# Kernel tuning notes

Measured on AMD Instinct MI355X. Metric: run time of the kernel, lower is better.

Reference implementation:

```python
import jax, jax.numpy as jnp
import numpy as np

D, E, N, DD, K = 1024, 2048, 16, 64, 4  # d_model, d_inner, d_state, dt_rank, d_conv
B, L = 2, 1024
EPS = 1e-5


def setup_inputs() -> dict:
    key = jax.random.key(0)
    ks = jax.random.split(key, 12)
    f = lambda k, s, scale=0.02: (jax.random.normal(k, s, jnp.float32) * scale)
    return dict(
        resid=jax.random.normal(ks[0], (B, L, D), jnp.float32),
        workplace_h=jnp.zeros((B, E, N), jnp.float32),
        norm_w=jnp.ones((D,), jnp.float32),
        skip_w=f(ks[1], (E, D)),
        in_w=f(ks[2], (E, D)),
        conv_w=f(ks[3], (E, 1, K), 0.2),
        conv_b=jnp.zeros((E,), jnp.float32),
        wd1=f(ks[4], (DD, E)),
        wd2_w=f(ks[5], (E, DD)),
        wd2_b=jnp.zeros((E,), jnp.float32),
        wb=f(ks[6], (N, E)),
        wc=f(ks[7], (N, E)),
        A_log=f(ks[8], (E, N), 1.0),
        W_D=jnp.ones((E,), jnp.float32),
        out_w=f(ks[9], (D, E)),
    )


def reference(resid, workplace_h, norm_w, skip_w, in_w, conv_w, conv_b,
              wd1, wd2_w, wd2_b, wb, wc, A_log, W_D, out_w):
    # RMSNorm
    x = resid * jax.lax.rsqrt(jnp.mean(resid ** 2, -1, keepdims=True) + EPS) * norm_w
    skip = x @ skip_w.T                      # [B,L,E]
    xi = x @ in_w.T                          # [B,L,E]
    # depthwise causal conv1d (torch pads both sides then slices to L; equivalent to left-pad K-1)
    xc = jnp.swapaxes(xi, 1, 2)              # [B,E,L]
    xc = jax.lax.conv_general_dilated(
        xc, conv_w, window_strides=(1,), padding=[(K - 1, 0)],
        feature_group_count=E, dimension_numbers=('NCH', 'OIH', 'NCH'))
    xc = xc + conv_b[None, :, None]
    x2 = jax.nn.silu(jnp.swapaxes(xc, 1, 2))  # [B,L,E]

    A = -jnp.exp(A_log)                       # [E,N]
    delta = jax.nn.softplus((x2 @ wd1.T) @ wd2_w.T + wd2_b)   # [B,L,E]
    A_bar = jnp.exp(delta[..., None] * A)                      # [B,L,E,N]
    Bm = x2 @ wb.T                                             # [B,L,N]
    B_bar = delta[..., None] * Bm[:, :, None, :]               # [B,L,E,N]
    Cm = x2 @ wc.T                                             # [B,L,N]

    def step(h, inp):
        a, b_, xl, cl = inp                   # [B,E,N],[B,E,N],[B,E],[B,N]
        h = a * h + b_ * xl[..., None]
        y = jnp.einsum('ben,bn->be', h, cl)
        return h, y

    h0 = jnp.zeros_like(workplace_h)          # workplace_h is zeroed (h[:] = 0)
    xs = (jnp.swapaxes(A_bar, 0, 1), jnp.swapaxes(B_bar, 0, 1),
          jnp.swapaxes(x2, 0, 1), jnp.swapaxes(Cm, 0, 1))
    _, ys = jax.lax.scan(step, h0, xs)        # ys: [L,B,E]
    y = jnp.swapaxes(ys, 0, 1)                # [B,L,E]

    y = (y + x2 * W_D) * jax.nn.silu(skip)
    return resid + y @ out_w.T
```

## Files before the change

### kernel.cpp

```cpp
#include <hip/hip_runtime.h>
#include <math.h>

#define Dm 1024
#define Em 2048
#define Nm 16
#define DDm 64
#define Bb 2
#define Lm 1024
#define Mrows (Bb*Lm)
#define NCH 32
#define CLEN 32
#define KS 16
#define KSO 4

typedef __attribute__((ext_vector_type(8))) short bf16x8;
typedef __attribute__((ext_vector_type(4))) float f32x4;
typedef unsigned int u32;
typedef unsigned short u16;

__device__ __forceinline__ u16 f2bf(float f) {
    union { float f; u32 u; } v; v.f = f;
    u32 r = v.u + 0x7fffu + ((v.u >> 16) & 1u);
    return (u16)(r >> 16);
}

__device__ __forceinline__ void async_copy16(const void* g, void* l) {
    __builtin_amdgcn_global_load_lds(
        (const __attribute__((address_space(1))) u32*)g,
        (__attribute__((address_space(3))) u32*)l,
        16, 0, 0);
}

__global__ __launch_bounds__(256) void rmsnorm_kernel(const float* __restrict__ resid,
                                                      const float* __restrict__ w,
                                                      u16* __restrict__ x) {
    int row = blockIdx.x;
    const float* r = resid + (size_t)row * Dm;
    float s = 0.f;
    for (int i = threadIdx.x; i < Dm; i += 256) { float v = r[i]; s += v * v; }
    __shared__ float red[4];
    for (int off = 32; off; off >>= 1) s += __shfl_down(s, off, 64);
    if ((threadIdx.x & 63) == 0) red[threadIdx.x >> 6] = s;
    __syncthreads();
    if (threadIdx.x == 0) {
        float t = red[0] + red[1] + red[2] + red[3];
        red[0] = rsqrtf(t / (float)Dm + 1e-5f);
    }
    __syncthreads();
    float sc = red[0];
    u16* xo = x + (size_t)row * Dm;
    for (int i = threadIdx.x; i < Dm; i += 256) xo[i] = f2bf(r[i] * sc * w[i]);
}

__global__ __launch_bounds__(256) void prep_all_kernel(const float* __restrict__ skip_w,
                                                       const float* __restrict__ in_w,
                                                       const float* __restrict__ out_w,
                                                       const float* __restrict__ wd2_w,
                                                       const float* __restrict__ wb,
                                                       const float* __restrict__ wc,
                                                       const float* __restrict__ wd1,
                                                       u16* __restrict__ skip_w_bf,
                                                       u16* __restrict__ in_w_bf,
                                                       u16* __restrict__ out_w_bf,
                                                       u16* __restrict__ wd2_bf,
                                                       u16* __restrict__ wtb) {
    const int R0 = 2097152, R1 = 4194304, R2 = 6291456, R3 = 6422528, R4 = 6684672;
    int i = blockIdx.x * 256 + threadIdx.x;
    if (i < R0) skip_w_bf[i] = f2bf(skip_w[i]);
    else if (i < R1) in_w_bf[i - R0] = f2bf(in_w[i - R0]);
    else if (i < R2) out_w_bf[i - R1] = f2bf(out_w[i - R1]);
    else if (i < R3) wd2_bf[i - R2] = f2bf(wd2_w[i - R2]);
    else if (i < R4) {
        int j = i - R3;
        int c = j >> 11, k = j & 2047;
        float v = 0.f;
        if (c < 16) v = wb[(size_t)c * Em + k];
        else if (c < 32) v = wc[(size_t)(c - 16) * Em + k];
        else if (c < 96) v = wd1[(size_t)(c - 32) * Em + k];
        wtb[j] = f2bf(v);
    }
}

__global__ __launch_bounds__(256) void gemm64(const u16* __restrict__ A,
                                              const u16* __restrict__ W,
                                              const float* __restrict__ bias,
                                              const float* __restrict__ addend,
                                              float* __restrict__ C,
                                              float* __restrict__ C2, int split,
                                              int M, int N, int lda, int klen, int act) {
    __shared__ __align__(16) u16 As[128 * 32];
    __shared__ __align__(16) u16 Ws[64 * 32];
    int tid = threadIdx.x;
    int lane = tid & 63, wave = tid >> 6;
    int bm = blockIdx.y * 128, bn = blockIdx.x * 64;
    int kbase = blockIdx.z * klen;
    int lm = lane & 15, lq = lane >> 4;
    int wm = (wave & 1) * 64, wn = (wave >> 1) * 32;

    f32x4 acc[4][2] = {};
    int ldrow = (lane >> 2);
    int ldchunk = (lane & 3) * 8;

    for (int k0 = kbase; k0 < kbase + klen; k0 += 32) {
        #pragma unroll
        for (int i = 0; i < 2; ++i) {
            int rbase = i * 64 + wave * 16;
            async_copy16(A + (size_t)(bm + rbase + ldrow) * lda + k0 + ldchunk, &As[rbase * 32]);
        }
        {
            int rbase = wave * 16;
            async_copy16(W + (size_t)(bn + rbase + ldrow) * lda + k0 + ldchunk, &Ws[rbase * 32]);
        }
        __syncthreads();
        bf16x8 a[4], b[2];
        #pragma unroll
        for (int mi = 0; mi < 4; ++mi)
            a[mi] = *(const bf16x8*)&As[(wm + mi * 16 + lm) * 32 + lq * 8];
        #pragma unroll
        for (int nj = 0; nj < 2; ++nj)
            b[nj] = *(const bf16x8*)&Ws[(wn + nj * 16 + lm) * 32 + lq * 8];
        #pragma unroll
        for (int mi = 0; mi < 4; ++mi)
            #pragma unroll
            for (int nj = 0; nj < 2; ++nj)
                acc[mi][nj] = __builtin_amdgcn_mfma_f32_16x16x32_bf16(a[mi], b[nj], acc[mi][nj], 0, 0, 0);
        __syncthreads();
    }

    int ldc = C2 ? split : N;
    float* Cz = C + (size_t)blockIdx.z * M * ldc;
    #pragma unroll
    for (int nj = 0; nj < 2; ++nj) {
        int col = bn + wn + nj * 16 + lm;
        float bv = bias ? bias[col] : 0.f;
        float* Cp = Cz; int colw = col;
        if (C2 && col >= split) { Cp = C2; colw = col - split; }
        #pragma unroll
        for (int mi = 0; mi < 4; ++mi) {
            #pragma unroll
            for (int r = 0; r < 4; ++r) {
                int row = bm + wm + mi * 16 + lq * 4 + r;
                float v = acc[mi][nj][r] + bv;
                if (act == 1) v = (v > 20.f) ? v : log1pf(expf(v));
                size_t off = (size_t)row * ldc + colw;
                if (addend) v += addend[off];
                Cp[off] = v;
            }
        }
    }
}

__global__ __launch_bounds__(256) void out_reduce_kernel(const float* __restrict__ part,
                                                         const float* __restrict__ resid,
                                                         float* __restrict__ out) {
    int idx = blockIdx.x * 256 + threadIdx.x;
    const float4* r4 = (const float4*)resid;
    const float4* p4 = (const float4*)part;
    float4 s = r4[idx];
    const int plane = Mrows * Dm / 4;
    #pragma unroll
    for (int ks = 0; ks < KSO; ++ks) {
        float4 p = p4[(size_t)ks * plane + idx];
        s.x += p.x; s.y += p.y; s.z += p.z; s.w += p.w;
    }
    ((float4*)out)[idx] = s;
}

__global__ __launch_bounds__(256) void small_gemm_mfma(const u16* __restrict__ A,
                                                       const u16* __restrict__ W,
                                                       float* __restrict__ Cp) {
    __shared__ __align__(16) u16 As[128 * 32];
    __shared__ __align__(16) u16 Ws[128 * 32];
    int tid = threadIdx.x;
    int lane = tid & 63, wave = tid >> 6;
    int bm = blockIdx.x * 128;
    int k0base = blockIdx.y * (Em / KS);
    int lm = lane & 15, lq = lane >> 4;
    int wm = (wave & 1) * 64, wn = (wave >> 1) * 64;

    f32x4 acc[4][4] = {};
    int ldrow = (lane >> 2);
    int ldchunk = (lane & 3) * 8;

    #pragma unroll
    for (int kk = 0; kk < (Em / KS) / 32; ++kk) {
        int k0 = k0base + kk * 32;
        #pragma unroll
        for (int i = 0; i < 2; ++i) {
            int rbase = i * 64 + wave * 16;
            async_copy16(A + (size_t)(bm + rbase + ldrow) * Em + k0 + ldchunk, &As[rbase * 32]);
            async_copy16(W + (size_t)(rbase + ldrow) * Em + k0 + ldchunk, &Ws[rbase * 32]);
        }
        __syncthreads();
        bf16x8 a[4], b[4];
        #pragma unroll
        for (int mi = 0; mi < 4; ++mi)
            a[mi] = *(const bf16x8*)&As[(wm + mi * 16 + lm) * 32 + lq * 8];
        #pragma unroll
        for (int nj = 0; nj < 4; ++nj)
            b[nj] = *(const bf16x8*)&Ws[(wn + nj * 16 + lm) * 32 + lq * 8];
        #pragma unroll
        for (int mi = 0; mi < 4; ++mi)
            #pragma unroll
            for (int nj = 0; nj < 4; ++nj)
                acc[mi][nj] = __builtin_amdgcn_mfma_f32_16x16x32_bf16(a[mi], b[nj], acc[mi][nj], 0, 0, 0);
        __syncthreads();
    }

    float* Co = Cp + (size_t)blockIdx.y * (Mrows * 128);
    #pragma unroll
    for (int nj = 0; nj < 4; ++nj) {
        int col = wn + nj * 16 + lm;
        #pragma unroll
        for (int mi = 0; mi < 4; ++mi) {
            #pragma unroll
            for (int r = 0; r < 4; ++r) {
                int row = bm + wm + mi * 16 + lq * 4 + r;
                Co[(size_t)row * 128 + col] = acc[mi][nj][r];
            }
        }
    }
}

__global__ __launch_bounds__(256) void small_reduce_kernel(const float* __restrict__ Cp,
                                                           float* __restrict__ Bm,
                                                           float* __restrict__ Cm,
                                                           u16* __restrict__ d1) {
    int idx = blockIdx.x * 256 + threadIdx.x;
    int row = idx >> 7, col = idx & 127;
    float s = 0.f;
    #pragma unroll
    for (int ks = 0; ks < KS; ++ks) s += Cp[(size_t)ks * (Mrows * 128) + idx];
    if (col < 16) Bm[(size_t)row * 16 + col] = s;
    else if (col < 32) Cm[(size_t)row * 16 + (col - 16)] = s;
    else if (col < 96) d1[(size_t)row * 64 + (col - 32)] = f2bf(s);
}

__global__ __launch_bounds__(256) void conv_silu_kernel(const float* __restrict__ xi,
                                                        const float* __restrict__ cw,
                                                        const float* __restrict__ cb,
                                                        float* __restrict__ x2,
                                                        u16* __restrict__ x2b, int total) {
    int idx = blockIdx.x * 256 + threadIdx.x;
    if (idx >= total) return;
    int e = idx & (Em - 1);
    int l = (idx >> 11) & (Lm - 1);
    const float* base = xi + idx;
    float w0 = cw[e * 4 + 0], w1 = cw[e * 4 + 1], w2 = cw[e * 4 + 2], w3 = cw[e * 4 + 3];
    float acc = cb[e];
    if (l >= 3) acc += w0 * base[-3 * Em];
    if (l >= 2) acc += w1 * base[-2 * Em];
    if (l >= 1) acc += w2 * base[-1 * Em];
    acc += w3 * base[0];
    float v = acc / (1.f + __expf(-acc));
    x2[idx] = v;
    x2b[idx] = f2bf(v);
}

__global__ __launch_bounds__(256) void scan1_kernel(const float* __restrict__ delta,
                                                    const float* __restrict__ x2,
                                                    const float* __restrict__ Bm,
                                                    const float* __restrict__ A_log,
                                                    float* __restrict__ h_end,
                                                    float* __restrict__ P) {
    int e = (blockIdx.x & 7) * 256 + threadIdx.x;
    int bc = blockIdx.x >> 3;
    int b = bc & 1, c = bc >> 1;
    float A[16];
    {
        const float4* al = (const float4*)(A_log + e * 16);
        float4 q0 = al[0], q1 = al[1], q2 = al[2], q3 = al[3];
        A[0]=-expf(q0.x); A[1]=-expf(q0.y); A[2]=-expf(q0.z); A[3]=-expf(q0.w);
        A[4]=-expf(q1.x); A[5]=-expf(q1.y); A[6]=-expf(q1.z); A[7]=-expf(q1.w);
        A[8]=-expf(q2.x); A[9]=-expf(q2.y); A[10]=-expf(q2.z); A[11]=-expf(q2.w);
        A[12]=-expf(q3.x); A[13]=-expf(q3.y); A[14]=-expf(q3.z); A[15]=-expf(q3.w);
    }
    float h[16], Pr[16];
    #pragma unroll
    for (int k = 0; k < 16; ++k) { h[k] = 0.f; Pr[k] = 1.f; }

    int l0 = c * CLEN;
    const float* dp = delta + ((size_t)(b * Lm + l0)) * Em + e;
    const float* xp = x2    + ((size_t)(b * Lm + l0)) * Em + e;
    const float* bp = Bm    + ((size_t)(b * Lm + l0)) * Nm;

    float d_n = dp[0], x_n = xp[0];
    float4 b0n = *(const float4*)(bp + 0), b1n = *(const float4*)(bp + 4);
    float4 b2n = *(const float4*)(bp + 8), b3n = *(const float4*)(bp + 12);

    #pragma unroll 1
    for (int l = 0; l < CLEN; ++l) {
        float d = d_n, xv = x_n;
        float4 b0 = b0n, b1 = b1n, b2 = b2n, b3 = b3n;
        if (l < CLEN - 1) {
            d_n = dp[(size_t)(l + 1) * Em]; x_n = xp[(size_t)(l + 1) * Em];
            const float* nb = bp + (size_t)(l + 1) * Nm;
            b0n = *(const float4*)(nb); b1n = *(const float4*)(nb + 4);
            b2n = *(const float4*)(nb + 8); b3n = *(const float4*)(nb + 12);
        }
        float dx = d * xv;
        float bb[16] = {b0.x,b0.y,b0.z,b0.w, b1.x,b1.y,b1.z,b1.w,
                        b2.x,b2.y,b2.z,b2.w, b3.x,b3.y,b3.z,b3.w};
        #pragma unroll
        for (int k = 0; k < 16; ++k) {
            float a = __expf(d * A[k]);
            h[k] = a * h[k] + bb[k] * dx;
            Pr[k] *= a;
        }
    }
    size_t base = (((size_t)c * 2 + b) * 16) * 2048 + e;
    #pragma unroll
    for (int k = 0; k < 16; ++k) {
        h_end[base + k * 2048] = h[k];
        P[base + k * 2048] = Pr[k];
    }
}

__global__ __launch_bounds__(256) void scan2_kernel(float* __restrict__ h_end,
                                                    const float* __restrict__ P) {
    int T = blockIdx.x * 256 + threadIdx.x;
    float hi = 0.f;
    float he_n = h_end[T], p_n = P[T];
    #pragma unroll 1
    for (int c = 0; c < NCH; ++c) {
        float he = he_n, p = p_n;
        if (c < NCH - 1) {
            he_n = h_end[(size_t)(c + 1) * 65536 + T];
            p_n  = P[(size_t)(c + 1) * 65536 + T];
        }
        float hnew = fmaf(p, hi, he);
        h_end[(size_t)c * 65536 + T] = hi;
        hi = hnew;
    }
}

__global__ __launch_bounds__(256) void scan3_kernel(const float* __restrict__ delta,
                                                    const float* __restrict__ x2,
                                                    const float* __restrict__ Bm,
                                                    const float* __restrict__ Cm,
                                                    const float* __restrict__ A_log,
                                                    const float* __restrict__ h_init,
                                                    const float* __restrict__ skip,
                                                    const float* __restrict__ W_D,
                                                    u16* __restrict__ yb) {
    int e = (blockIdx.x & 7) * 256 + threadIdx.x;
    int bc = blockIdx.x >> 3;
    int b = bc & 1, c = bc >> 1;
    float A[16];
    {
        const float4* al = (const float4*)(A_log + e * 16);
        float4 q0 = al[0], q1 = al[1], q2 = al[2], q3 = al[3];
        A[0]=-expf(q0.x); A[1]=-expf(q0.y); A[2]=-expf(q0.z); A[3]=-expf(q0.w);
        A[4]=-expf(q1.x); A[5]=-expf(q1.y); A[6]=-expf(q1.z); A[7]=-expf(q1.w);
        A[8]=-expf(q2.x); A[9]=-expf(q2.y); A[10]=-expf(q2.z); A[11]=-expf(q2.w);
        A[12]=-expf(q3.x); A[13]=-expf(q3.y); A[14]=-expf(q3.z); A[15]=-expf(q3.w);
    }
    float h[16];
    {
        size_t base = (((size_t)c * 2 + b) * 16) * 2048 + e;
        #pragma unroll
        for (int k = 0; k < 16; ++k) h[k] = h_init[base + k * 2048];
    }
    float wd = W_D[e];

    int l0 = c * CLEN;
    const float* dp = delta + ((size_t)(b * Lm + l0)) * Em + e;
    const float* xp = x2    + ((size_t)(b * Lm + l0)) * Em + e;
    const float* sp = skip  + ((size_t)(b * Lm + l0)) * Em + e;
    const float* bp = Bm    + ((size_t)(b * Lm + l0)) * Nm;
    const float* cp = Cm    + ((size_t)(b * Lm + l0)) * Nm;
    u16* yp = yb + ((size_t)(b * Lm + l0)) * Em + e;

    float d_n = dp[0], x_n = xp[0], s_n = sp[0];
    float4 b0n = *(const float4*)(bp + 0), b1n = *(const float4*)(bp + 4);
    float4 b2n = *(const float4*)(bp + 8), b3n = *(const float4*)(bp + 12);
    float4 c0n = *(const float4*)(cp + 0), c1n = *(const float4*)(cp + 4);
    float4 c2n = *(const float4*)(cp + 8), c3n = *(const float4*)(cp + 12);

    #pragma unroll 1
    for (int l = 0; l < CLEN; ++l) {
        float d = d_n, xv = x_n, sv = s_n;
        float4 b0 = b0n, b1 = b1n, b2 = b2n, b3 = b3n;
        float4 c0 = c0n, c1 = c1n, c2 = c2n, c3 = c3n;
        if (l < CLEN - 1) {
            d_n = dp[(size_t)(l + 1) * Em]; x_n = xp[(size_t)(l + 1) * Em];
            s_n = sp[(size_t)(l + 1) * Em];
            const float* nb = bp + (size_t)(l + 1) * Nm;
            b0n = *(const float4*)(nb); b1n = *(const float4*)(nb + 4);
            b2n = *(const float4*)(nb + 8); b3n = *(const float4*)(nb + 12);
            const float* nc = cp + (size_t)(l + 1) * Nm;
            c0n = *(const float4*)(nc); c1n = *(const float4*)(nc + 4);
            c2n = *(const float4*)(nc + 8); c3n = *(const float4*)(nc + 12);
        }
        float dx = d * xv;
        float bb[16] = {b0.x,b0.y,b0.z,b0.w, b1.x,b1.y,b1.z,b1.w,
                        b2.x,b2.y,b2.z,b2.w, b3.x,b3.y,b3.z,b3.w};
        float cc[16] = {c0.x,c0.y,c0.z,c0.w, c1.x,c1.y,c1.z,c1.w,
                        c2.x,c2.y,c2.z,c2.w, c3.x,c3.y,c3.z,c3.w};
        float yv = 0.f;
        #pragma unroll
        for (int k = 0; k < 16; ++k) {
            float a = __expf(d * A[k]);
            h[k] = a * h[k] + bb[k] * dx;
            yv += h[k] * cc[k];
        }
        float sig = 1.f / (1.f + __expf(-sv));
        yp[(size_t)l * Em] = f2bf((yv + xv * wd) * (sv * sig));
    }
}

extern "C" void kernel_launch(void* const* d_in, const int* in_sizes, int n_in,
                              void* d_out, int out_size, void* d_ws, size_t ws_size,
                              hipStream_t stream) {
    const float* resid  = (const float*)d_in[0];
    const float* norm_w = (const float*)d_in[2];
    const float* skip_w = (const float*)d_in[3];
    const float* in_w   = (const float*)d_in[4];
    const float* conv_w = (const float*)d_in[5];
    const float* conv_b = (const float*)d_in[6];
    const float* wd1    = (const float*)d_in[7];
    const float* wd2_w  = (const float*)d_in[8];
    const float* wd2_b  = (const float*)d_in[9];
    const float* wb     = (const float*)d_in[10];
    const float* wc     = (const float*)d_in[11];
    const float* A_log  = (const float*)d_in[12];
    const float* W_D    = (const float*)d_in[13];
    const float* out_w  = (const float*)d_in[14];
    float* out = (float*)d_out;

    float* ws = (float*)d_ws;
    float* region0 = ws; ws += 3 * 1024 * 1024;
    u16* x_bf      = (u16*)region0;
    u16* skip_w_bf = (u16*)(region0 + 1024 * 1024);
    u16* in_w_bf   = (u16*)(region0 + 2 * 1024 * 1024);
    float* h_endb  = region0;
    u16* out_w_bf  = (u16*)ws; ws += 1024 * 1024;
    u16* wd2_bf    = (u16*)ws; ws += 65536;
    u16* d1_bf     = (u16*)ws; ws += 65536;
    u16* wtb       = (u16*)ws; ws += 131072;
    float* Pbuf    = ws; ws += 2 * 1024 * 1024;
    float* Cpart   = ws; ws += (size_t)KS * Mrows * 128;
    float* skip    = ws; ws += (size_t)Mrows * Em;
    float* xi      = ws; ws += (size_t)Mrows * Em;
    float* x2      = ws; ws += (size_t)Mrows * Em;
    u16* x2_bf     = (u16*)ws; ws += (size_t)Mrows * Em / 2;
    u16* yb_bf     = (u16*)ws; ws += (size_t)Mrows * Em / 2;
    float* Bmb     = ws; ws += (size_t)Mrows * Nm;
    float* Cmb     = ws; ws += (size_t)Mrows * Nm;
    float* delta   = xi;
    float* OutPart = skip;

    const int M = Mrows;

    prep_all_kernel<<<6684672 / 256, 256, 0, stream>>>(
        skip_w, in_w, out_w, wd2_w, wb, wc, wd1,
        skip_w_bf, in_w_bf, out_w_bf, wd2_bf, wtb);

    rmsnorm_kernel<<<M, 256, 0, stream>>>(resid, norm_w, x_bf);

    gemm64<<<dim3(2 * Em / 64, M / 128, 1), 256, 0, stream>>>(
        x_bf, skip_w_bf, nullptr, nullptr, skip, xi, Em, M, 2 * Em, Dm, Dm, 0);

    conv_silu_kernel<<<(M * Em) / 256, 256, 0, stream>>>(xi, conv_w, conv_b, x2, x2_bf, M * Em);

    small_gemm_mfma<<<dim3(M / 128, KS), 256, 0, stream>>>(x2_bf, wtb, Cpart);
    small_reduce_kernel<<<(M * 128) / 256, 256, 0, stream>>>(Cpart, Bmb, Cmb, d1_bf);

    gemm64<<<dim3(Em / 64, M / 128, 1), 256, 0, stream>>>(
        d1_bf, wd2_bf, wd2_b, nullptr, delta, nullptr, 0, M, Em, DDm, DDm, 1);

    scan1_kernel<<<Bb * NCH * 8, 256, 0, stream>>>(delta, x2, Bmb, A_log, h_endb, Pbuf);
    scan2_kernel<<<65536 / 256, 256, 0, stream>>>(h_endb, Pbuf);
    scan3_kernel<<<Bb * NCH * 8, 256, 0, stream>>>(delta, x2, Bmb, Cmb, A_log, h_endb,
                                                   skip, W_D, yb_bf);

    gemm64<<<dim3(Dm / 64, M / 128, KSO), 256, 0, stream>>>(
        yb_bf, out_w_bf, nullptr, nullptr, OutPart, nullptr, 0, M, Dm, Em, Em / KSO, 0);
    out_reduce_kernel<<<(M * Dm / 4) / 256, 256, 0, stream>>>(OutPart, resid, out);
}
```

Before: 280.1 us.

## Use 128x128 GEMM tiles and XOR-swizzle LDS layout to avoid bank conflicts

Adds a gemm128 kernel with 128x128 output tiles (4x4 MFMA per wave) for the in/skip projection and the output projection, which doubles operand reuse per LDS load. All MFMA GEMMs also XOR-swizzle the 16-byte chunk position within each LDS row, on both the async global-to-LDS copy and the fragment reads, to cut LDS bank conflicts. The small delta GEMM keeps 128x64 tiles in a slimmed-down kernel. Larger tiles halve the block count and raise register pressure, which may lower occupancy; the out projection grid drops to 8x16x4 blocks.

```diff
diff --git a/kernel.cpp b/kernel.cpp
--- a/kernel.cpp
+++ b/kernel.cpp
@@ -81,48 +81,47 @@
     }
 }
 
-__global__ __launch_bounds__(256) void gemm64(const u16* __restrict__ A,
-                                              const u16* __restrict__ W,
-                                              const float* __restrict__ bias,
-                                              const float* __restrict__ addend,
-                                              float* __restrict__ C,
-                                              float* __restrict__ C2, int split,
-                                              int M, int N, int lda, int klen, int act) {
+
+__global__ __launch_bounds__(256) void gemm128(const u16* __restrict__ A,
+                                               const u16* __restrict__ W,
+                                               const float* __restrict__ bias,
+                                               const float* __restrict__ addend,
+                                               float* __restrict__ C,
+                                               float* __restrict__ C2, int split,
+                                               int M, int N, int lda, int klen, int act) {
     __shared__ __align__(16) u16 As[128 * 32];
-    __shared__ __align__(16) u16 Ws[64 * 32];
+    __shared__ __align__(16) u16 Ws[128 * 32];
     int tid = threadIdx.x;
     int lane = tid & 63, wave = tid >> 6;
-    int bm = blockIdx.y * 128, bn = blockIdx.x * 64;
+    int bm = blockIdx.y * 128, bn = blockIdx.x * 128;
     int kbase = blockIdx.z * klen;
     int lm = lane & 15, lq = lane >> 4;
-    int wm = (wave & 1) * 64, wn = (wave >> 1) * 32;
-
-    f32x4 acc[4][2] = {};
-    int ldrow = (lane >> 2);
-    int ldchunk = (lane & 3) * 8;
+    int wm = (wave & 1) * 64, wn = (wave >> 1) * 64;
+
+    f32x4 acc[4][4] = {};
+    int ldrow = lane >> 2;
+    int gchunk = ((lane & 3) ^ ((lane >> 3) & 3)) * 8;
+    int psw = (lm >> 1) & 3;
 
     for (int k0 = kbase; k0 < kbase + klen; k0 += 32) {
         #pragma unroll
         for (int i = 0; i < 2; ++i) {
             int rbase = i * 64 + wave * 16;
-            async_copy16(A + (size_t)(bm + rbase + ldrow) * lda + k0 + ldchunk, &As[rbase * 32]);
-        }
-        {
-            int rbase = wave * 16;
-            async_copy16(W + (size_t)(bn + rbase + ldrow) * lda + k0 + ldchunk, &Ws[rbase * 32]);
+            async_copy16(A + (size_t)(bm + rbase + ldrow) * lda + k0 + gchunk, &As[rbase * 32]);
+            async_copy16(W + (size_t)(bn + rbase + ldrow) * lda + k0 + gchunk, &Ws[rbase * 32]);
         }
         __syncthreads();
-        bf16x8 a[4], b[2];
+        bf16x8 a[4], b[4];
         #pragma unroll
         for (int mi = 0; mi < 4; ++mi)
-            a[mi] = *(const bf16x8*)&As[(wm + mi * 16 + lm) * 32 + lq * 8];
-        #pragma unroll
-        for (int nj = 0; nj < 2; ++nj)
-            b[nj] = *(const bf16x8*)&Ws[(wn + nj * 16 + lm) * 32 + lq * 8];
+            a[mi] = *(const bf16x8*)&As[(wm + mi * 16 + lm) * 32 + (lq ^ psw) * 8];
+        #pragma unroll
+        for (int nj = 0; nj < 4; ++nj)
+            b[nj] = *(const bf16x8*)&Ws[(wn + nj * 16 + lm) * 32 + (lq ^ psw) * 8];
         #pragma unroll
         for (int mi = 0; mi < 4; ++mi)
             #pragma unroll
-            for (int nj = 0; nj < 2; ++nj)
+            for (int nj = 0; nj < 4; ++nj)
                 acc[mi][nj] = __builtin_amdgcn_mfma_f32_16x16x32_bf16(a[mi], b[nj], acc[mi][nj], 0, 0, 0);
         __syncthreads();
     }
@@ -130,7 +129,7 @@
     int ldc = C2 ? split : N;
     float* Cz = C + (size_t)blockIdx.z * M * ldc;
     #pragma unroll
-    for (int nj = 0; nj < 2; ++nj) {
+    for (int nj = 0; nj < 4; ++nj) {
         int col = bn + wn + nj * 16 + lm;
         float bv = bias ? bias[col] : 0.f;
         float* Cp = Cz; int colw = col;
@@ -145,6 +144,67 @@
                 size_t off = (size_t)row * ldc + colw;
                 if (addend) v += addend[off];
                 Cp[off] = v;
+            }
+        }
+    }
+}
+
+__global__ __launch_bounds__(256) void gemm64(const u16* __restrict__ A,
+                                              const u16* __restrict__ W,
+                                              const float* __restrict__ bias,
+                                              float* __restrict__ C,
+                                              int M, int N, int lda, int klen, int act) {
+    __shared__ __align__(16) u16 As[128 * 32];
+    __shared__ __align__(16) u16 Ws[64 * 32];
+    int tid = threadIdx.x;
+    int lane = tid & 63, wave = tid >> 6;
+    int bm = blockIdx.y * 128, bn = blockIdx.x * 64;
+    int lm = lane & 15, lq = lane >> 4;
+    int wm = (wave & 1) * 64, wn = (wave >> 1) * 32;
+
+    f32x4 acc[4][2] = {};
+    int ldrow = lane >> 2;
+    int gchunk = ((lane & 3) ^ ((lane >> 3) & 3)) * 8;
+    int psw = (lm >> 1) & 3;
+
+    for (int k0 = 0; k0 < klen; k0 += 32) {
+        #pragma unroll
+        for (int i = 0; i < 2; ++i) {
+            int rbase = i * 64 + wave * 16;
+            async_copy16(A + (size_t)(bm + rbase + ldrow) * lda + k0 + gchunk, &As[rbase * 32]);
+        }
+        {
+            int rbase = wave * 16;
+            async_copy16(W + (size_t)(bn + rbase + ldrow) * lda + k0 + gchunk, &Ws[rbase * 32]);
+        }
+        __syncthreads();
+        bf16x8 a[4], b[2];
+        #pragma unroll
+        for (int mi = 0; mi < 4; ++mi)
+            a[mi] = *(const bf16x8*)&As[(wm + mi * 16 + lm) * 32 + (lq ^ psw) * 8];
+        #pragma unroll
+        for (int nj = 0; nj < 2; ++nj)
+            b[nj] = *(const bf16x8*)&Ws[(wn + nj * 16 + lm) * 32 + (lq ^ psw) * 8];
+        #pragma unroll
+        for (int mi = 0; mi < 4; ++mi)
+            #pragma unroll
+            for (int nj = 0; nj < 2; ++nj)
+                acc[mi][nj] = __builtin_amdgcn_mfma_f32_16x16x32_bf16(a[mi], b[nj], acc[mi][nj], 0, 0, 0);
+        __syncthreads();
+    }
+
+    #pragma unroll
+    for (int nj = 0; nj < 2; ++nj) {
+        int col = bn + wn + nj * 16 + lm;
+        float bv = bias ? bias[col] : 0.f;
+        #pragma unroll
+        for (int mi = 0; mi < 4; ++mi) {
+            #pragma unroll
+            for (int r = 0; r < 4; ++r) {
+                int row = bm + wm + mi * 16 + lq * 4 + r;
+                float v = acc[mi][nj][r] + bv;
+                if (act == 1) v = (v > 20.f) ? v : log1pf(expf(v));
+                C[(size_t)row * N + col] = v;
             }
         }
     }
@@ -179,8 +239,9 @@
     int wm = (wave & 1) * 64, wn = (wave >> 1) * 64;
 
     f32x4 acc[4][4] = {};
-    int ldrow = (lane >> 2);
-    int ldchunk = (lane & 3) * 8;
+    int ldrow = lane >> 2;
+    int gchunk = ((lane & 3) ^ ((lane >> 3) & 3)) * 8;
+    int psw = (lm >> 1) & 3;
 
     #pragma unroll
     for (int kk = 0; kk < (Em / KS) / 32; ++kk) {
@@ -188,17 +249,17 @@
         #pragma unroll
         for (int i = 0; i < 2; ++i) {
             int rbase = i * 64 + wave * 16;
-            async_copy16(A + (size_t)(bm + rbase + ldrow) * Em + k0 + ldchunk, &As[rbase * 32]);
-            async_copy16(W + (size_t)(rbase + ldrow) * Em + k0 + ldchunk, &Ws[rbase * 32]);
+            async_copy16(A + (size_t)(bm + rbase + ldrow) * Em + k0 + gchunk, &As[rbase * 32]);
+            async_copy16(W + (size_t)(rbase + ldrow) * Em + k0 + gchunk, &Ws[rbase * 32]);
         }
         __syncthreads();
         bf16x8 a[4], b[4];
         #pragma unroll
         for (int mi = 0; mi < 4; ++mi)
-            a[mi] = *(const bf16x8*)&As[(wm + mi * 16 + lm) * 32 + lq * 8];
+            a[mi] = *(const bf16x8*)&As[(wm + mi * 16 + lm) * 32 + (lq ^ psw) * 8];
         #pragma unroll
         for (int nj = 0; nj < 4; ++nj)
-            b[nj] = *(const bf16x8*)&Ws[(wn + nj * 16 + lm) * 32 + lq * 8];
+            b[nj] = *(const bf16x8*)&Ws[(wn + nj * 16 + lm) * 32 + (lq ^ psw) * 8];
         #pragma unroll
         for (int mi = 0; mi < 4; ++mi)
             #pragma unroll
@@ -458,7 +519,7 @@
 
     rmsnorm_kernel<<<M, 256, 0, stream>>>(resid, norm_w, x_bf);
 
-    gemm64<<<dim3(2 * Em / 64, M / 128, 1), 256, 0, stream>>>(
+    gemm128<<<dim3(2 * Em / 128, M / 128, 1), 256, 0, stream>>>(
         x_bf, skip_w_bf, nullptr, nullptr, skip, xi, Em, M, 2 * Em, Dm, Dm, 0);
 
     conv_silu_kernel<<<(M * Em) / 256, 256, 0, stream>>>(xi, conv_w, conv_b, x2, x2_bf, M * Em);
@@ -466,15 +527,15 @@
     small_gemm_mfma<<<dim3(M / 128, KS), 256, 0, stream>>>(x2_bf, wtb, Cpart);
     small_reduce_kernel<<<(M * 128) / 256, 256, 0, stream>>>(Cpart, Bmb, Cmb, d1_bf);
 
-    gemm64<<<dim3(Em / 64, M / 128, 1), 256, 0, stream>>>(
-        d1_bf, wd2_bf, wd2_b, nullptr, delta, nullptr, 0, M, Em, DDm, DDm, 1);
+    gemm64<<<dim3(Em / 64, M / 128), 256, 0, stream>>>(
+        d1_bf, wd2_bf, wd2_b, delta, M, Em, DDm, DDm, 1);
 
     scan1_kernel<<<Bb * NCH * 8, 256, 0, stream>>>(delta, x2, Bmb, A_log, h_endb, Pbuf);
     scan2_kernel<<<65536 / 256, 256, 0, stream>>>(h_endb, Pbuf);
     scan3_kernel<<<Bb * NCH * 8, 256, 0, stream>>>(delta, x2, Bmb, Cmb, A_log, h_endb,
                                                    skip, W_D, yb_bf);
 
-    gemm64<<<dim3(Dm / 64, M / 128, KSO), 256, 0, stream>>>(
+    gemm128<<<dim3(Dm / 128, M / 128, KSO), 256, 0, stream>>>(
         yb_bf, out_w_bf, nullptr, nullptr, OutPart, nullptr, 0, M, Dm, Em, Em / KSO, 0);
     out_reduce_kernel<<<(M * Dm / 4) / 256, 256, 0, stream>>>(OutPart, resid, out);
 }
```

Measured after the change: 300.4 us. 7.2% more time.

## Double-buffer GEMM LDS tiles with XOR swizzle and unify small GEMM path

Applied to the files above, without the earlier changes.

Replaces the single-buffered gemm64 with gemm_db. gemm_db keeps two LDS stages, so the next K-slice's async copies are issued while MFMAs run on the current slice, and it uses an XOR-swizzled chunk layout to reduce LDS bank conflicts. The dedicated small_gemm_mfma kernel for the B/C/dt projections is dropped in favour of the same gemm_db with a split-K grid, and the unused addend path is removed. This doubles LDS per block, which may reduce occupancy. Correctness depends on the async copies being complete before the loop-end barrier.

```diff
diff --git a/kernel.cpp b/kernel.cpp
--- a/kernel.cpp
+++ b/kernel.cpp
@@ -81,15 +81,14 @@
     }
 }
 
-__global__ __launch_bounds__(256) void gemm64(const u16* __restrict__ A,
-                                              const u16* __restrict__ W,
-                                              const float* __restrict__ bias,
-                                              const float* __restrict__ addend,
-                                              float* __restrict__ C,
-                                              float* __restrict__ C2, int split,
-                                              int M, int N, int lda, int klen, int act) {
-    __shared__ __align__(16) u16 As[128 * 32];
-    __shared__ __align__(16) u16 Ws[64 * 32];
+__global__ __launch_bounds__(256) void gemm_db(const u16* __restrict__ A,
+                                               const u16* __restrict__ W,
+                                               const float* __restrict__ bias,
+                                               float* __restrict__ C,
+                                               float* __restrict__ C2, int split,
+                                               int M, int N, int lda, int klen, int act) {
+    __shared__ __align__(16) u16 As[2][128 * 32];
+    __shared__ __align__(16) u16 Ws[2][64 * 32];
     int tid = threadIdx.x;
     int lane = tid & 63, wave = tid >> 6;
     int bm = blockIdx.y * 128, bn = blockIdx.x * 64;
@@ -98,27 +97,39 @@
     int wm = (wave & 1) * 64, wn = (wave >> 1) * 32;
 
     f32x4 acc[4][2] = {};
-    int ldrow = (lane >> 2);
-    int ldchunk = (lane & 3) * 8;
-
-    for (int k0 = kbase; k0 < kbase + klen; k0 += 32) {
-        #pragma unroll
-        for (int i = 0; i < 2; ++i) {
-            int rbase = i * 64 + wave * 16;
-            async_copy16(A + (size_t)(bm + rbase + ldrow) * lda + k0 + ldchunk, &As[rbase * 32]);
-        }
-        {
-            int rbase = wave * 16;
-            async_copy16(W + (size_t)(bn + rbase + ldrow) * lda + k0 + ldchunk, &Ws[rbase * 32]);
-        }
-        __syncthreads();
+    int ldrow = lane >> 2;
+    int gchunk = ((lane & 3) ^ ((lane >> 3) & 3)) * 8;
+    int psw = (lm >> 1) & 3;
+    int rdoff = (lq ^ psw) * 8;
+
+    const u16* Arow0 = A + (size_t)(bm + wave * 16 + ldrow) * lda + gchunk;
+    const u16* Arow1 = A + (size_t)(bm + 64 + wave * 16 + ldrow) * lda + gchunk;
+    const u16* Wrow  = W + (size_t)(bn + wave * 16 + ldrow) * lda + gchunk;
+    int ldsA = (wave * 16) * 32;
+    int ldsA2 = (64 + wave * 16) * 32;
+    int ldsW = (wave * 16) * 32;
+
+    int nIter = klen / 32;
+    async_copy16(Arow0 + kbase, &As[0][ldsA]);
+    async_copy16(Arow1 + kbase, &As[0][ldsA2]);
+    async_copy16(Wrow + kbase, &Ws[0][ldsW]);
+    __syncthreads();
+
+    for (int it = 0; it < nIter; ++it) {
+        int cur = it & 1, nxt = cur ^ 1;
+        if (it + 1 < nIter) {
+            int k0 = kbase + (it + 1) * 32;
+            async_copy16(Arow0 + k0, &As[nxt][ldsA]);
+            async_copy16(Arow1 + k0, &As[nxt][ldsA2]);
+            async_copy16(Wrow + k0, &Ws[nxt][ldsW]);
+        }
         bf16x8 a[4], b[2];
         #pragma unroll
         for (int mi = 0; mi < 4; ++mi)
-            a[mi] = *(const bf16x8*)&As[(wm + mi * 16 + lm) * 32 + lq * 8];
+            a[mi] = *(const bf16x8*)&As[cur][(wm + mi * 16 + lm) * 32 + rdoff];
         #pragma unroll
         for (int nj = 0; nj < 2; ++nj)
-            b[nj] = *(const bf16x8*)&Ws[(wn + nj * 16 + lm) * 32 + lq * 8];
+            b[nj] = *(const bf16x8*)&Ws[cur][(wn + nj * 16 + lm) * 32 + rdoff];
         #pragma unroll
         for (int mi = 0; mi < 4; ++mi)
             #pragma unroll
@@ -142,9 +153,7 @@
                 int row = bm + wm + mi * 16 + lq * 4 + r;
                 float v = acc[mi][nj][r] + bv;
                 if (act == 1) v = (v > 20.f) ? v : log1pf(expf(v));
-                size_t off = (size_t)row * ldc + colw;
-                if (addend) v += addend[off];
-                Cp[off] = v;
+                Cp[(size_t)row * ldc + colw] = v;
             }
         }
     }
@@ -164,62 +173,6 @@
         s.x += p.x; s.y += p.y; s.z += p.z; s.w += p.w;
     }
     ((float4*)out)[idx] = s;
-}
-
-__global__ __launch_bounds__(256) void small_gemm_mfma(const u16* __restrict__ A,
-                                                       const u16* __restrict__ W,
-                                                       float* __restrict__ Cp) {
-    __shared__ __align__(16) u16 As[128 * 32];
-    __shared__ __align__(16) u16 Ws[128 * 32];
-    int tid = threadIdx.x;
-    int lane = tid & 63, wave = tid >> 6;
-    int bm = blockIdx.x * 128;
-    int k0base = blockIdx.y * (Em / KS);
-    int lm = lane & 15, lq = lane >> 4;
-    int wm = (wave & 1) * 64, wn = (wave >> 1) * 64;
-
-    f32x4 acc[4][4] = {};
-    int ldrow = (lane >> 2);
-    int ldchunk = (lane & 3) * 8;
-
-    #pragma unroll
-    for (int kk = 0; kk < (Em / KS) / 32; ++kk) {
-        int k0 = k0base + kk * 32;
-        #pragma unroll
-        for (int i = 0; i < 2; ++i) {
-            int rbase = i * 64 + wave * 16;
-            async_copy16(A + (size_t)(bm + rbase + ldrow) * Em + k0 + ldchunk, &As[rbase * 32]);
-            async_copy16(W + (size_t)(rbase + ldrow) * Em + k0 + ldchunk, &Ws[rbase * 32]);
-        }
-        __syncthreads();
-        bf16x8 a[4], b[4];
-        #pragma unroll
-        for (int mi = 0; mi < 4; ++mi)
-            a[mi] = *(const bf16x8*)&As[(wm + mi * 16 + lm) * 32 + lq * 8];
-        #pragma unroll
-        for (int nj = 0; nj < 4; ++nj)
-            b[nj] = *(const bf16x8*)&Ws[(wn + nj * 16 + lm) * 32 + lq * 8];
-        #pragma unroll
-        for (int mi = 0; mi < 4; ++mi)
-            #pragma unroll
-            for (int nj = 0; nj < 4; ++nj)
-                acc[mi][nj] = __builtin_amdgcn_mfma_f32_16x16x32_bf16(a[mi], b[nj], acc[mi][nj], 0, 0, 0);
-        __syncthreads();
-    }
-
-    float* Co = Cp + (size_t)blockIdx.y * (Mrows * 128);
-    #pragma unroll
-    for (int nj = 0; nj < 4; ++nj) {
-        int col = wn + nj * 16 + lm;
-        #pragma unroll
-        for (int mi = 0; mi < 4; ++mi) {
-            #pragma unroll
-            for (int r = 0; r < 4; ++r) {
-                int row = bm + wm + mi * 16 + lq * 4 + r;
-                Co[(size_t)row * 128 + col] = acc[mi][nj][r];
-            }
-        }
-    }
 }
 
 __global__ __launch_bounds__(256) void small_reduce_kernel(const float* __restrict__ Cp,
@@ -458,23 +411,24 @@
 
     rmsnorm_kernel<<<M, 256, 0, stream>>>(resid, norm_w, x_bf);
 
-    gemm64<<<dim3(2 * Em / 64, M / 128, 1), 256, 0, stream>>>(
-        x_bf, skip_w_bf, nullptr, nullptr, skip, xi, Em, M, 2 * Em, Dm, Dm, 0);
+    gemm_db<<<dim3(2 * Em / 64, M / 128, 1), 256, 0, stream>>>(
+        x_bf, skip_w_bf, nullptr, skip, xi, Em, M, 2 * Em, Dm, Dm, 0);
 
     conv_silu_kernel<<<(M * Em) / 256, 256, 0, stream>>>(xi, conv_w, conv_b, x2, x2_bf, M * Em);
 
-    small_gemm_mfma<<<dim3(M / 128, KS), 256, 0, stream>>>(x2_bf, wtb, Cpart);
+    gemm_db<<<dim3(128 / 64, M / 128, KS), 256, 0, stream>>>(
+        x2_bf, wtb, nullptr, Cpart, nullptr, 0, M, 128, Em, Em / KS, 0);
     small_reduce_kernel<<<(M * 128) / 256, 256, 0, stream>>>(Cpart, Bmb, Cmb, d1_bf);
 
-    gemm64<<<dim3(Em / 64, M / 128, 1), 256, 0, stream>>>(
-        d1_bf, wd2_bf, wd2_b, nullptr, delta, nullptr, 0, M, Em, DDm, DDm, 1);
+    gemm_db<<<dim3(Em / 64, M / 128, 1), 256, 0, stream>>>(
+        d1_bf, wd2_bf, wd2_b, delta, nullptr, 0, M, Em, DDm, DDm, 1);
 
     scan1_kernel<<<Bb * NCH * 8, 256, 0, stream>>>(delta, x2, Bmb, A_log, h_endb, Pbuf);
     scan2_kernel<<<65536 / 256, 256, 0, stream>>>(h_endb, Pbuf);
     scan3_kernel<<<Bb * NCH * 8, 256, 0, stream>>>(delta, x2, Bmb, Cmb, A_log, h_endb,
                                                    skip, W_D, yb_bf);
 
-    gemm64<<<dim3(Dm / 64, M / 128, KSO), 256, 0, stream>>>(
-        yb_bf, out_w_bf, nullptr, nullptr, OutPart, nullptr, 0, M, Dm, Em, Em / KSO, 0);
+    gemm_db<<<dim3(Dm / 64, M / 128, KSO), 256, 0, stream>>>(
+        yb_bf, out_w_bf, nullptr, OutPart, nullptr, 0, M, Dm, Em, Em / KSO, 0);
     out_reduce_kernel<<<(M * Dm / 4) / 256, 256, 0, stream>>>(OutPart, resid, out);
 }
```

Measured after the change: 274.0 us. 2.2% less time.
